# Performance work log

Measured on AMD Instinct MI355X. Metric: run time of the kernel, lower is better.

Reference implementation:

```python
import jax, jax.numpy as jnp
import numpy as np


def qdq(x):
    """Per-tensor symmetric int8 quantize-dequantize (act_quant + fp8_gemm dequant semantics)."""
    scale = jnp.maximum(jnp.max(jnp.abs(x)) / 127.0, 1e-8)
    q = jnp.clip(jnp.round(x / scale), -127.0, 127.0) * scale
    # straight-through estimator so the reference is also usable under autodiff
    return x + jax.lax.stop_gradient(q - x)


def layernorm(x, scale, bias, eps=1e-6):
    mean = jnp.mean(x, axis=-1, keepdims=True)
    var = jnp.mean(jnp.square(x - mean), axis=-1, keepdims=True)
    return (x - mean) * jax.lax.rsqrt(var + eps) * scale + bias


def glin(t, W, b):
    """TPUGEMMLinear: quantized GEMM (dequantized matmul) + bias."""
    return jnp.matmul(qdq(t), qdq(W)) + b


def setup_inputs() -> dict:
    key = jax.random.key(0)
    ks = jax.random.split(key, 12)
    B, S, D = 4, 1024, 1024
    H, HD, F, P = 32, 32, 4096, 32
    lecun = lambda k, shape: jax.random.normal(k, shape, jnp.float32) * (1.0 / np.sqrt(shape[0]))
    return {
        'inputs': jax.random.normal(ks[0], (B, S, D), jnp.float32),
        'ln1_scale': jnp.ones((D,), jnp.float32),
        'ln1_bias': jnp.zeros((D,), jnp.float32),
        'Wq': lecun(ks[1], (D, H * HD)), 'bq': jnp.zeros((H * HD,), jnp.float32),
        'Wk': lecun(ks[2], (D, H * HD)), 'bk': jnp.zeros((H * HD,), jnp.float32),
        'Wv': lecun(ks[3], (D, H * HD)), 'bv': jnp.zeros((H * HD,), jnp.float32),
        'rel_pos_emb': jax.random.normal(ks[4], (2 * P + 1, HD), jnp.float32) * 0.02,
        'Wo': lecun(ks[5], (H * HD, D)), 'bo': jnp.zeros((D,), jnp.float32),
        'ln2_scale': jnp.ones((D,), jnp.float32),
        'ln2_bias': jnp.zeros((D,), jnp.float32),
        'W1': lecun(ks[6], (D, F)), 'b1': jnp.zeros((F,), jnp.float32),
        'W2': lecun(ks[7], (F, D)), 'b2': jnp.zeros((D,), jnp.float32),
    }


def reference(inputs, ln1_scale, ln1_bias, Wq, bq, Wk, bk, Wv, bv, rel_pos_emb,
              Wo, bo, ln2_scale, ln2_bias, W1, b1, W2, b2):
    B, S, D = inputs.shape
    HD = rel_pos_emb.shape[1]
    H = D // HD
    P = (rel_pos_emb.shape[0] - 1) // 2

    # Pre-attention LayerNorm (TPULayerNorm, eps=1e-6)
    x = layernorm(inputs, ln1_scale, ln1_bias)

    # Quantized QKV projections
    q = glin(x, Wq, bq).reshape(B, S, H, HD).transpose(0, 2, 1, 3)  # [B,H,S,HD]
    k = glin(x, Wk, bk).reshape(B, S, H, HD).transpose(0, 2, 1, 3)
    v = glin(x, Wv, bv).reshape(B, S, H, HD).transpose(0, 2, 1, 3)

    # Relative position bias: [1, HD, S, S] broadcast onto head axis (HD == H by construction)
    pos = jnp.clip(jnp.arange(S)[:, None] - jnp.arange(S)[None, :] + P, 0, 2 * P)
    rel_bias = rel_pos_emb[pos].transpose(2, 0, 1)[None]  # [1, HD, S, S]

    # Quantized content scores + bias, custom scale factor
    scores = jnp.einsum('bhqd,bhkd->bhqk', qdq(q), qdq(k)) + rel_bias
    scale = jnp.sqrt(jnp.asarray(HD, jnp.float32)) * jnp.power(jnp.asarray(S, jnp.float32), 0.25)
    scores = scores / scale

    # Stable softmax with +1e-6 denominator (as in source)
    m = jnp.max(scores, axis=-1, keepdims=True)
    e = jnp.exp(scores - m)
    w = e / (jnp.sum(e, axis=-1, keepdims=True) + 1e-6)

    attn = jnp.einsum('bhqk,bhkd->bhqd', w, qdq(v))  # values quantized, weights not
    attn = attn.transpose(0, 2, 1, 3).reshape(B, S, H * HD)
    attn_out = glin(attn, Wo, bo)

    xr = attn_out + inputs
    y = layernorm(xr, ln2_scale, ln2_bias)

    # MLP (_mlp_tpu assumed: quantized Linear -> gelu -> quantized Linear)
    h = jax.nn.gelu(glin(y, W1, b1))
    out = glin(h, W2, b2)
    # NOTE: source returns mlp_output directly (no second residual add)
    return out
```

## Files before the change

### kernel.cpp

```cpp
#include <hip/hip_runtime.h>
#include <cstdint>


typedef unsigned short u16;
typedef __bf16 bf16x4 __attribute__((ext_vector_type(4)));
typedef __bf16 bf16x8 __attribute__((ext_vector_type(8)));
typedef float  f32x4  __attribute__((ext_vector_type(4)));

#define MFMA(a, b, c) __builtin_amdgcn_mfma_f32_16x16x32_bf16(a, b, c, 0, 0, 0)

#define NSLOT 13
#define PSPREAD 64
#define PSTRIDE 16
#define SLOTSZ (PSPREAD * PSTRIDE)

__device__ __forceinline__ float bf2f(u16 h) {
    return __uint_as_float(((unsigned)h) << 16);
}
__device__ __forceinline__ u16 f2bf(float f) {
    unsigned u = __float_as_uint(f);
    u += 0x7FFFu + ((u >> 16) & 1u);
    return (u16)(u >> 16);
}
__device__ __forceinline__ float qdqv(float v, float s) {
    float q = rintf(v / s);
    q = fminf(fmaxf(q, -127.f), 127.f);
    return q * s;
}

__device__ __forceinline__ float getscale64(const int* scales, int slot) {
    float m = __int_as_float(scales[slot * SLOTSZ + (threadIdx.x & 63) * PSTRIDE]);
#pragma unroll
    for (int o = 32; o > 0; o >>= 1) m = fmaxf(m, __shfl_xor(m, o));
    return fmaxf(m / 127.f, 1e-8f);
}

typedef const __attribute__((address_space(1))) unsigned gas_u32;
typedef __attribute__((address_space(3))) unsigned las_u32;
__device__ __forceinline__ void gld16(const void* g, void* l) {
    __builtin_amdgcn_global_load_lds((gas_u32*)g, (las_u32*)l, 16, 0, 0);
}

__global__ void zero_k(int* s) {
    const int i = blockIdx.x * 256 + threadIdx.x;
    if (i < NSLOT * SLOTSZ) s[i] = 0;
}

__global__ __launch_bounds__(256) void wabsmax6_k(const float* __restrict__ w0, const float* __restrict__ w1,
                                                  const float* __restrict__ w2, const float* __restrict__ w3,
                                                  const float* __restrict__ w4, const float* __restrict__ w5,
                                                  int* scales) {
    const int b = blockIdx.x;
    int ti, boff;
    if (b < 1024)      { ti = b >> 8; boff = (b & 255) * 4096; }
    else if (b < 2048) { ti = 4;      boff = (b - 1024) * 4096; }
    else               { ti = 5;      boff = (b - 2048) * 4096; }
    const float* w = (ti == 0) ? w0 : (ti == 1) ? w1 : (ti == 2) ? w2
                   : (ti == 3) ? w3 : (ti == 4) ? w4 : w5;
    const float4* wv = (const float4*)(w + boff);
    float m = 0.f;
#pragma unroll
    for (int k = 0; k < 4; k++) {
        float4 v = wv[threadIdx.x + k * 256];
        m = fmaxf(m, fmaxf(fmaxf(fabsf(v.x), fabsf(v.y)), fmaxf(fabsf(v.z), fabsf(v.w))));
    }
#pragma unroll
    for (int o = 32; o > 0; o >>= 1) m = fmaxf(m, __shfl_xor(m, o));
    if ((threadIdx.x & 63) == 0)
        atomicMax(scales + (7 + ti) * SLOTSZ + (((b * 4 + (threadIdx.x >> 6)) & (PSPREAD - 1)) * PSTRIDE),
                  __float_as_int(m));
}

__global__ __launch_bounds__(256) void wqt6_k(const float* __restrict__ w0, const float* __restrict__ w1,
                                              const float* __restrict__ w2, const float* __restrict__ w3,
                                              const float* __restrict__ w4, const float* __restrict__ w5,
                                              u16* __restrict__ wtbase, const int* __restrict__ scales) {
    __shared__ float t[32][33];
    const int b = blockIdx.x;
    const float* W;
    u16* Wt;
    int K, N, bx, by, slot;
    if (b < 4096) {
        const int ti = b >> 10, r = b & 1023;
        W = (ti == 0) ? w0 : (ti == 1) ? w1 : (ti == 2) ? w2 : w3;
        Wt = wtbase + (long)ti * 1048576;
        K = 1024; N = 1024; bx = r & 31; by = r >> 5; slot = 7 + ti;
    } else if (b < 8192) {
        const int r = b - 4096;
        W = w4; Wt = wtbase + 4194304;
        K = 1024; N = 4096; bx = r & 127; by = r >> 7; slot = 11;
    } else {
        const int r = b - 8192;
        W = w5; Wt = wtbase + 8388608;
        K = 4096; N = 1024; bx = r & 31; by = r >> 5; slot = 12;
    }
    const int n0 = bx * 32, k0 = by * 32;
    const float s = getscale64(scales, slot);
    const int c = threadIdx.x & 31, r0 = threadIdx.x >> 5;
#pragma unroll
    for (int i = 0; i < 4; i++) {
        int kk = k0 + r0 + i * 8;
        t[r0 + i * 8][c] = qdqv(W[(long)kk * N + n0 + c], s);
    }
    __syncthreads();
#pragma unroll
    for (int i = 0; i < 4; i++) {
        int nn = n0 + r0 + i * 8;
        Wt[(long)nn * K + k0 + c] = f2bf(t[c][r0 + i * 8]);
    }
}

__device__ __forceinline__ float blk_sum(float v, float* red) {
#pragma unroll
    for (int o = 32; o > 0; o >>= 1) v += __shfl_xor(v, o);
    __syncthreads();
    if ((threadIdx.x & 63) == 0) red[threadIdx.x >> 6] = v;
    __syncthreads();
    return red[0] + red[1] + red[2] + red[3];
}

__device__ __forceinline__ void blk_absmax_commit(float am, float* red, int* scales, int slot) {
#pragma unroll
    for (int o = 32; o > 0; o >>= 1) am = fmaxf(am, __shfl_xor(am, o));
    __syncthreads();
    if ((threadIdx.x & 63) == 0) red[threadIdx.x >> 6] = am;
    __syncthreads();
    if (threadIdx.x == 0) {
        float m = fmaxf(fmaxf(red[0], red[1]), fmaxf(red[2], red[3]));
        atomicMax(scales + slot * SLOTSZ + ((blockIdx.x & (PSPREAD - 1)) * PSTRIDE),
                  __float_as_int(m));
    }
}

__global__ __launch_bounds__(256) void ln_k(const float* __restrict__ in, const float* __restrict__ gam,
                                            const float* __restrict__ bet, u16* __restrict__ out,
                                            int* __restrict__ scales, int slot) {
    __shared__ float red[4];
    const long row = blockIdx.x;
    const int tid = threadIdx.x;
    float4 v = ((const float4*)(in + row * 1024))[tid];
    float mean = blk_sum(v.x + v.y + v.z + v.w, red) * (1.f / 1024.f);
    float dx = v.x - mean, dy = v.y - mean, dz = v.z - mean, dw = v.w - mean;
    float var = blk_sum(dx * dx + dy * dy + dz * dz + dw * dw, red) * (1.f / 1024.f);
    float inv = rsqrtf(var + 1e-6f);
    float4 gg = ((const float4*)gam)[tid];
    float4 bb = ((const float4*)bet)[tid];
    float o0 = dx * inv * gg.x + bb.x, o1 = dy * inv * gg.y + bb.y;
    float o2 = dz * inv * gg.z + bb.z, o3 = dw * inv * gg.w + bb.w;
    ushort4 st;
    st.x = f2bf(o0); st.y = f2bf(o1); st.z = f2bf(o2); st.w = f2bf(o3);
    ((ushort4*)(out + row * 1024))[tid] = st;
    float am = fmaxf(fmaxf(fabsf(o0), fabsf(o1)), fmaxf(fabsf(o2), fabsf(o3)));
    blk_absmax_commit(am, red, scales, slot);
}

__global__ __launch_bounds__(256) void ln2comb_k(const float* __restrict__ p, const float* __restrict__ bo,
                                                 const float* __restrict__ inputs,
                                                 const float* __restrict__ gam, const float* __restrict__ bet,
                                                 u16* __restrict__ out, int* __restrict__ scales) {
    __shared__ float red[4];
    const long row = blockIdx.x;
    const int tid = threadIdx.x;
    float4 a = ((const float4*)(p + row * 1024))[tid];
    float4 b = ((const float4*)(p + 4194304 + row * 1024))[tid];
    float4 bb0 = ((const float4*)bo)[tid];
    float4 xi = ((const float4*)(inputs + row * 1024))[tid];
    float4 v;
    v.x = a.x + b.x + bb0.x + xi.x; v.y = a.y + b.y + bb0.y + xi.y;
    v.z = a.z + b.z + bb0.z + xi.z; v.w = a.w + b.w + bb0.w + xi.w;
    float mean = blk_sum(v.x + v.y + v.z + v.w, red) * (1.f / 1024.f);
    float dx = v.x - mean, dy = v.y - mean, dz = v.z - mean, dw = v.w - mean;
    float var = blk_sum(dx * dx + dy * dy + dz * dz + dw * dw, red) * (1.f / 1024.f);
    float inv = rsqrtf(var + 1e-6f);
    float4 gg = ((const float4*)gam)[tid];
    float4 bb = ((const float4*)bet)[tid];
    float o0 = dx * inv * gg.x + bb.x, o1 = dy * inv * gg.y + bb.y;
    float o2 = dz * inv * gg.z + bb.z, o3 = dw * inv * gg.w + bb.w;
    ushort4 st;
    st.x = f2bf(o0); st.y = f2bf(o1); st.z = f2bf(o2); st.w = f2bf(o3);
    ((ushort4*)(out + row * 1024))[tid] = st;
    float am = fmaxf(fmaxf(fabsf(o0), fabsf(o1)), fmaxf(fabsf(o2), fabsf(o3)));
    blk_absmax_commit(am, red, scales, 5);
}

__global__ void combo_k(const float* __restrict__ p, const float* __restrict__ b2,
                        float* __restrict__ out) {
    const int i = blockIdx.x * 256 + threadIdx.x;
    float4 a = ((const float4*)p)[i];
    float4 b = ((const float4*)(p + 4194304))[i];
    float4 bb = ((const float4*)b2)[i & 255];
    float4 o;
    o.x = a.x + b.x + bb.x; o.y = a.y + b.y + bb.y;
    o.z = a.z + b.z + bb.z; o.w = a.w + b.w + bb.w;
    ((float4*)out)[i] = o;
}

__global__ void qact_k(u16* buf, int n8, const int* __restrict__ scales, int slot) {
    const float s = getscale64(scales, slot);
    int i = blockIdx.x * 256 + threadIdx.x;
    if (i >= n8) return;
    uint4 u = ((const uint4*)buf)[i];
    unsigned w[4] = {u.x, u.y, u.z, u.w};
#pragma unroll
    for (int j = 0; j < 4; j++) {
        float lo = qdqv(bf2f((u16)(w[j] & 0xFFFFu)), s);
        float hi = qdqv(bf2f((u16)(w[j] >> 16)), s);
        w[j] = (unsigned)f2bf(lo) | ((unsigned)f2bf(hi) << 16);
    }
    uint4 o; o.x = w[0]; o.y = w[1]; o.z = w[2]; o.w = w[3];
    ((uint4*)buf)[i] = o;
}

__global__ void qact2_k(u16* buf, const int* __restrict__ scales) {
    const int i = blockIdx.x * 256 + threadIdx.x;
    const int slot = (i >= 524288) ? 2 : 1;
    const float s = getscale64(scales, slot);
    uint4 u = ((const uint4*)buf)[i];
    unsigned w[4] = {u.x, u.y, u.z, u.w};
#pragma unroll
    for (int j = 0; j < 4; j++) {
        float lo = qdqv(bf2f((u16)(w[j] & 0xFFFFu)), s);
        float hi = qdqv(bf2f((u16)(w[j] >> 16)), s);
        w[j] = (unsigned)f2bf(lo) | ((unsigned)f2bf(hi) << 16);
    }
    uint4 o; o.x = w[0]; o.y = w[1]; o.z = w[2]; o.w = w[3];
    ((uint4*)buf)[i] = o;
}

__global__ __launch_bounds__(256) void vtrans_k(const u16* __restrict__ v, u16* __restrict__ vt,
                                                const int* __restrict__ scales) {
    __shared__ u16 t[32][33];
    const int bh = blockIdx.y, s0 = blockIdx.x * 32;
    const float s = getscale64(scales, 3);
    const int c = threadIdx.x & 31, r0 = threadIdx.x >> 5;
    const u16* src = v + ((long)bh * 1024 + s0) * 32;
#pragma unroll
    for (int i = 0; i < 4; i++) {
        int r = r0 + i * 8;
        t[r][c] = f2bf(qdqv(bf2f(src[r * 32 + c]), s));
    }
    __syncthreads();
    u16* dst = vt + (long)bh * 32768;
#pragma unroll
    for (int i = 0; i < 4; i++) {
        int r = r0 + i * 8;
        dst[(long)r * 1024 + s0 + c] = t[c][r];
    }
}

template <int EPI>
__global__ __launch_bounds__(256, 2) void gemm_k(const u16* __restrict__ A, const u16* __restrict__ Bt,
                                                 const float* __restrict__ bias, const float* __restrict__ bias2,
                                                 const float* __restrict__ bias3,
                                                 int M, int N, int Kfull, int Kslice,
                                                 float* __restrict__ outf, u16* __restrict__ outb,
                                                 int* __restrict__ scales, int slot) {
    __shared__ u16 As[128 * 64];
    __shared__ u16 Bs[128 * 64];
    const float* bp = bias;
    long koff = 0, ooff = 0;
    if (EPI == 0) {
        const int z = blockIdx.z;
        Bt += (long)z * 1048576;
        outb += (long)z * 4194304;
        bp = (z == 0) ? bias : (z == 1 ? bias2 : bias3);
        slot += z;
    }
    if (EPI == 4) {
        koff = (long)blockIdx.z * Kslice * 2;
        ooff = (long)blockIdx.z * M * N;
    }
    const int tid = threadIdx.x;
    const int lane = tid & 63;
    const int wave = tid >> 6;
    const int wm = wave >> 1, wn = wave & 1;
    const int bm = blockIdx.y * 128, bn = blockIdx.x * 128;
    const int g = lane >> 4, c = lane & 15;

    const long astride = (long)Kfull * 2;
    const int srow = wave * 32 + (lane >> 3);
    const int scol = ((lane & 7) * 16) ^ ((lane >> 3) << 4);
    const char* Ag = (const char*)A + (long)(bm + srow) * astride + scol + koff;
    const char* Bg = (const char*)Bt + (long)(bn + srow) * astride + scol + koff;
    char* Al = (char*)As + wave * 4096;
    char* Bl = (char*)Bs + wave * 4096;

    f32x4 acc[4][4];
    const f32x4 zf = {0.f, 0.f, 0.f, 0.f};
#pragma unroll
    for (int i = 0; i < 4; i++)
#pragma unroll
        for (int j = 0; j < 4; j++) acc[i][j] = zf;

    const int nk = Kslice >> 6;
    for (int kt = 0; kt < nk; ++kt) {
        __syncthreads();
        const long ko = (long)kt * 128;
#pragma unroll
        for (int i = 0; i < 4; i++) gld16(Ag + ko + (long)(i * 8) * astride, Al + i * 1024);
#pragma unroll
        for (int i = 0; i < 4; i++) gld16(Bg + ko + (long)(i * 8) * astride, Bl + i * 1024);
        __syncthreads();

#pragma unroll
        for (int kh = 0; kh < 2; kh++) {
            bf16x8 af[4], bq[4];
            const int kb = kh * 64 + g * 16;
            const int sw = kb ^ ((c & 7) << 4);
#pragma unroll
            for (int i = 0; i < 4; i++)
                af[i] = *(const bf16x8*)((const char*)As + (wm * 64 + i * 16 + c) * 128 + sw);
#pragma unroll
            for (int j = 0; j < 4; j++)
                bq[j] = *(const bf16x8*)((const char*)Bs + (wn * 64 + j * 16 + c) * 128 + sw);
#pragma unroll
            for (int i = 0; i < 4; i++)
#pragma unroll
                for (int j = 0; j < 4; j++)
                    acc[i][j] = MFMA(af[i], bq[j], acc[i][j]);
        }
    }

    float am = 0.f;
#pragma unroll
    for (int i = 0; i < 4; i++) {
#pragma unroll
        for (int j = 0; j < 4; j++) {
#pragma unroll
            for (int t = 0; t < 4; t++) {
                const int row = bm + wm * 64 + i * 16 + g * 4 + t;
                const int col = bn + wn * 64 + j * 16 + c;
                if (EPI == 0) {
                    float v = acc[i][j][t] + bp[col];
                    long oi = ((long)((row >> 10) * 32 + (col >> 5))) * 32768
                              + (long)(row & 1023) * 32 + (col & 31);
                    outb[oi] = f2bf(v);
                    am = fmaxf(am, fabsf(v));
                } else if (EPI == 2) {
                    float v = acc[i][j][t] + bp[col];
                    float t3 = v * v * v;
                    float gl = 0.5f * v * (1.f + tanhf(0.79788456080286536f * (v + 0.044715f * t3)));
                    outb[(long)row * N + col] = f2bf(gl);
                    am = fmaxf(am, fabsf(gl));
                } else {
                    outf[ooff + (long)row * N + col] = acc[i][j][t];
                }
            }
        }
    }
    if (EPI == 0 || EPI == 2) {
#pragma unroll
        for (int o = 32; o > 0; o >>= 1) am = fmaxf(am, __shfl_xor(am, o));
        if (lane == 0)
            atomicMax(scales + slot * SLOTSZ
                          + ((((blockIdx.x + blockIdx.y * gridDim.x) * 4 + wave) & (PSPREAD - 1)) * PSTRIDE),
                      __float_as_int(am));
    }
}

__global__ __launch_bounds__(256) void attn_k(const u16* __restrict__ q, const u16* __restrict__ k,
                                              const u16* __restrict__ vt, const float* __restrict__ relpos,
                                              u16* __restrict__ attn, int* __restrict__ scales) {
    __shared__ float rel_s[65];
    __shared__ u16 P[4][32 * 40];
    __shared__ float frs[4][32];
    const int tid = threadIdx.x;
    const int lane = tid & 63;
    const int w = tid >> 6;
    const int bh = blockIdx.x;
    const int b = bh >> 5, h = bh & 31;
    const int q0 = blockIdx.y * 128 + w * 32;
    const int g = lane >> 4, c = lane & 15;
    const float SC = 0.03125f;
    for (int i = tid; i < 65; i += 256) rel_s[i] = relpos[i * 32 + h] * SC;
    __syncthreads();
    const float rb0 = rel_s[0], rb64 = rel_s[64];

    const u16* qb = q + ((long)bh * 1024 + q0) * 32;
    const u16* kb = k + (long)bh * 32768;
    const u16* vb = vt + (long)bh * 32768;
    u16* Pw = P[w];
    float* fw = frs[w];

    bf16x8 aq[2];
#pragma unroll
    for (int i = 0; i < 2; i++) aq[i] = *(const bf16x8*)(qb + (i * 16 + c) * 32 + g * 8);

    const f32x4 zf = {0.f, 0.f, 0.f, 0.f};
    f32x4 o[2][2] = {{zf, zf}, {zf, zf}};
    float m_run[2] = {-1e30f, -1e30f};
    float l_run[2] = {0.f, 0.f};

    for (int kt = 0; kt < 32; ++kt) {
        const int kk = kt * 32;
        bf16x8 bk0 = *(const bf16x8*)(kb + (kk + c) * 32 + g * 8);
        bf16x8 bk1 = *(const bf16x8*)(kb + (kk + 16 + c) * 32 + g * 8);
        bf16x8 bv0 = *(const bf16x8*)(vb + c * 1024 + kk + g * 8);
        bf16x8 bv1 = *(const bf16x8*)(vb + (16 + c) * 1024 + kk + g * 8);
        const int mode = (kk >= q0 + 64) ? 0 : (kk <= q0 - 64) ? 1 : 2;

        float frv[2];
#pragma unroll
        for (int i = 0; i < 2; i++) {
            f32x4 s0 = MFMA(bk0, aq[i], zf);
            f32x4 s1 = MFMA(bk1, aq[i], zf);
            float v[8];
            if (mode == 0) {
#pragma unroll
                for (int t = 0; t < 4; t++) { v[t] = fmaf(s0[t], SC, rb0); v[4 + t] = fmaf(s1[t], SC, rb0); }
            } else if (mode == 1) {
#pragma unroll
                for (int t = 0; t < 4; t++) { v[t] = fmaf(s0[t], SC, rb64); v[4 + t] = fmaf(s1[t], SC, rb64); }
            } else {
                const int base = (q0 + i * 16 + c) - kk - g * 4 + 32;
#pragma unroll
                for (int t = 0; t < 4; t++) {
                    int d0 = min(max(base - t, 0), 64);
                    int d1 = min(max(base - 16 - t, 0), 64);
                    v[t] = fmaf(s0[t], SC, rel_s[d0]);
                    v[4 + t] = fmaf(s1[t], SC, rel_s[d1]);
                }
            }
            float mt = fmaxf(fmaxf(fmaxf(v[0], v[1]), fmaxf(v[2], v[3])),
                             fmaxf(fmaxf(v[4], v[5]), fmaxf(v[6], v[7])));
            mt = fmaxf(mt, __shfl_xor(mt, 16));
            mt = fmaxf(mt, __shfl_xor(mt, 32));
            const float mn = fmaxf(m_run[i], mt);
            const float fr = __expf(m_run[i] - mn);
            frv[i] = fr;
            float sm = 0.f;
            bf16x4 pk0, pk1;
#pragma unroll
            for (int t = 0; t < 4; t++) {
                float p = __expf(v[t] - mn);     sm += p; pk0[t] = (__bf16)p;
                float p2 = __expf(v[4 + t] - mn); sm += p2; pk1[t] = (__bf16)p2;
            }
            sm += __shfl_xor(sm, 16);
            sm += __shfl_xor(sm, 32);
            l_run[i] = l_run[i] * fr + sm;
            m_run[i] = mn;
            *(bf16x4*)&Pw[(i * 16 + c) * 40 + g * 4] = pk0;
            *(bf16x4*)&Pw[(i * 16 + c) * 40 + 16 + g * 4] = pk1;
        }
        if (__any((frv[0] != 1.f) | (frv[1] != 1.f))) {
            if (g == 0) { fw[c] = frv[0]; fw[16 + c] = frv[1]; }
            float4 f0 = *(float4*)&fw[g * 4];
            float4 f1 = *(float4*)&fw[16 + g * 4];
#pragma unroll
            for (int j = 0; j < 2; j++) {
                o[0][j][0] *= f0.x; o[0][j][1] *= f0.y; o[0][j][2] *= f0.z; o[0][j][3] *= f0.w;
                o[1][j][0] *= f1.x; o[1][j][1] *= f1.y; o[1][j][2] *= f1.z; o[1][j][3] *= f1.w;
            }
        }
        bf16x8 ap0 = *(const bf16x8*)&Pw[c * 40 + g * 8];
        bf16x8 ap1 = *(const bf16x8*)&Pw[(16 + c) * 40 + g * 8];
        o[0][0] = MFMA(ap0, bv0, o[0][0]);
        o[0][1] = MFMA(ap0, bv1, o[0][1]);
        o[1][0] = MFMA(ap1, bv0, o[1][0]);
        o[1][1] = MFMA(ap1, bv1, o[1][1]);
    }

    if (g == 0) { fw[c] = l_run[0]; fw[16 + c] = l_run[1]; }
    float4 l0 = *(float4*)&fw[g * 4];
    float4 l1 = *(float4*)&fw[16 + g * 4];
    float lv[2][4] = {{l0.x, l0.y, l0.z, l0.w}, {l1.x, l1.y, l1.z, l1.w}};
    float am = 0.f;
#pragma unroll
    for (int i = 0; i < 2; i++)
#pragma unroll
        for (int j = 0; j < 2; j++)
#pragma unroll
            for (int t = 0; t < 4; t++) {
                float val = o[i][j][t] / (lv[i][t] + 1e-6f);
                long row = (long)b * 1024 + q0 + i * 16 + g * 4 + t;
                attn[row * 1024 + h * 32 + j * 16 + c] = f2bf(val);
                am = fmaxf(am, fabsf(val));
            }
#pragma unroll
    for (int o2 = 32; o2 > 0; o2 >>= 1) am = fmaxf(am, __shfl_xor(am, o2));
    if (lane == 0)
        atomicMax(scales + 4 * SLOTSZ + ((((bh * 8 + blockIdx.y) * 4 + w) & (PSPREAD - 1)) * PSTRIDE),
                  __float_as_int(am));
}

extern "C" void kernel_launch(void* const* d_in, const int* in_sizes, int n_in,
                              void* d_out, int out_size, void* d_ws, size_t ws_size,
                              hipStream_t stream) {
    (void)in_sizes; (void)n_in; (void)out_size; (void)ws_size;
    const float* inputs = (const float*)d_in[0];
    const float* ln1s   = (const float*)d_in[1];
    const float* ln1b   = (const float*)d_in[2];
    const float* Wq     = (const float*)d_in[3];
    const float* bq     = (const float*)d_in[4];
    const float* Wk     = (const float*)d_in[5];
    const float* bk     = (const float*)d_in[6];
    const float* Wv     = (const float*)d_in[7];
    const float* bv     = (const float*)d_in[8];
    const float* rel    = (const float*)d_in[9];
    const float* Wo     = (const float*)d_in[10];
    const float* bo     = (const float*)d_in[11];
    const float* ln2s   = (const float*)d_in[12];
    const float* ln2b   = (const float*)d_in[13];
    const float* W1     = (const float*)d_in[14];
    const float* b1     = (const float*)d_in[15];
    const float* W2     = (const float*)d_in[16];
    const float* b2     = (const float*)d_in[17];
    float* out = (float*)d_out;

    char* ws = (char*)d_ws;
    int* scales = (int*)ws;
    char* regionA = ws + 65536;
    char* regionB = regionA + (32u << 20);
    char* regionC = regionB + (32u << 20);
    u16* qb    = (u16*)regionA;
    u16* kbuf  = qb + 4194304;
    u16* vbuf  = kbuf + 4194304;
    u16* vtb   = vbuf + 4194304;
    float* pWo = (float*)regionA;
    u16* hb    = (u16*)regionA;
    u16* xq    = (u16*)regionB;
    u16* attnb = xq;
    u16* yb    = xq + 4194304;
    float* pW2 = (float*)regionB;
    u16* wtb   = (u16*)regionC;

    zero_k<<<52, 256, 0, stream>>>(scales);
    wabsmax6_k<<<3072, 256, 0, stream>>>(Wq, Wk, Wv, Wo, W1, W2, scales);

    ln_k<<<4096, 256, 0, stream>>>(inputs, ln1s, ln1b, xq, scales, 0);

    wqt6_k<<<12288, 256, 0, stream>>>(Wq, Wk, Wv, Wo, W1, W2, wtb, scales);

    qact_k<<<2048, 256, 0, stream>>>(xq, 524288, scales, 0);

    gemm_k<0><<<dim3(8, 32, 3), 256, 0, stream>>>(xq, wtb, bq, bk, bv, 4096, 1024, 1024, 1024,
                                                  nullptr, qb, scales, 1);

    qact2_k<<<4096, 256, 0, stream>>>(qb, scales);
    vtrans_k<<<dim3(32, 128), 256, 0, stream>>>(vbuf, vtb, scales);

    attn_k<<<dim3(128, 8), 256, 0, stream>>>(qb, kbuf, vtb, rel, attnb, scales);
    qact_k<<<2048, 256, 0, stream>>>(attnb, 524288, scales, 4);

    gemm_k<4><<<dim3(8, 32, 2), 256, 0, stream>>>(attnb, wtb + 3145728, nullptr, nullptr, nullptr,
                                                  4096, 1024, 1024, 512, pWo, nullptr, scales, -1);
    ln2comb_k<<<4096, 256, 0, stream>>>(pWo, bo, inputs, ln2s, ln2b, yb, scales);
    qact_k<<<2048, 256, 0, stream>>>(yb, 524288, scales, 5);

    gemm_k<2><<<dim3(32, 32), 256, 0, stream>>>(yb, wtb + 4194304, b1, nullptr, nullptr,
                                                4096, 4096, 1024, 1024, nullptr, hb, scales, 6);
    qact_k<<<8192, 256, 0, stream>>>(hb, 2097152, scales, 6);

    gemm_k<4><<<dim3(8, 32, 2), 256, 0, stream>>>(hb, wtb + 8388608, nullptr, nullptr, nullptr,
                                                  4096, 1024, 4096, 2048, pW2, nullptr, scales, -1);
    combo_k<<<4096, 256, 0, stream>>>(pW2, b2, out);
}
```

Baseline: 315.6 us.

## Fuse small prologue kernels, split W2 GEMM four ways, shrink attention row tiles

Merges the weight-absmax kernel with the LN1 kernel, and the Q/K requantize kernel with the V quantize-transpose kernel, to cut launch count and tail effects. Splits the final W2 GEMM into four K-slices instead of two. The extra partial sums go to freed workspace and to the output buffer, and the combine kernel sums all four. Attention now gives each wave 16 query rows instead of 32 and launches twice as many blocks with a higher occupancy hint. This raises parallelism but halves K/V reuse per wave and adds more loads per MFMA.

Measured after the change: 345.2 us. 9.4% more time.

```diff
diff --git a/kernel.cpp b/kernel.cpp
--- a/kernel.cpp
+++ b/kernel.cpp
@@ -46,29 +46,74 @@
     if (i < NSLOT * SLOTSZ) s[i] = 0;
 }
 
-__global__ __launch_bounds__(256) void wabsmax6_k(const float* __restrict__ w0, const float* __restrict__ w1,
-                                                  const float* __restrict__ w2, const float* __restrict__ w3,
-                                                  const float* __restrict__ w4, const float* __restrict__ w5,
-                                                  int* scales) {
-    const int b = blockIdx.x;
-    int ti, boff;
-    if (b < 1024)      { ti = b >> 8; boff = (b & 255) * 4096; }
-    else if (b < 2048) { ti = 4;      boff = (b - 1024) * 4096; }
-    else               { ti = 5;      boff = (b - 2048) * 4096; }
-    const float* w = (ti == 0) ? w0 : (ti == 1) ? w1 : (ti == 2) ? w2
-                   : (ti == 3) ? w3 : (ti == 4) ? w4 : w5;
-    const float4* wv = (const float4*)(w + boff);
-    float m = 0.f;
-#pragma unroll
-    for (int k = 0; k < 4; k++) {
-        float4 v = wv[threadIdx.x + k * 256];
-        m = fmaxf(m, fmaxf(fmaxf(fabsf(v.x), fabsf(v.y)), fmaxf(fabsf(v.z), fabsf(v.w))));
-    }
-#pragma unroll
-    for (int o = 32; o > 0; o >>= 1) m = fmaxf(m, __shfl_xor(m, o));
-    if ((threadIdx.x & 63) == 0)
-        atomicMax(scales + (7 + ti) * SLOTSZ + (((b * 4 + (threadIdx.x >> 6)) & (PSPREAD - 1)) * PSTRIDE),
+__device__ __forceinline__ float blk_sum(float v, float* red) {
+#pragma unroll
+    for (int o = 32; o > 0; o >>= 1) v += __shfl_xor(v, o);
+    __syncthreads();
+    if ((threadIdx.x & 63) == 0) red[threadIdx.x >> 6] = v;
+    __syncthreads();
+    return red[0] + red[1] + red[2] + red[3];
+}
+
+__device__ __forceinline__ void blk_absmax_commit(float am, float* red, int* scales,
+                                                  int slot, int bidx) {
+#pragma unroll
+    for (int o = 32; o > 0; o >>= 1) am = fmaxf(am, __shfl_xor(am, o));
+    __syncthreads();
+    if ((threadIdx.x & 63) == 0) red[threadIdx.x >> 6] = am;
+    __syncthreads();
+    if (threadIdx.x == 0) {
+        float m = fmaxf(fmaxf(red[0], red[1]), fmaxf(red[2], red[3]));
+        atomicMax(scales + slot * SLOTSZ + ((bidx & (PSPREAD - 1)) * PSTRIDE),
                   __float_as_int(m));
+    }
+}
+
+__global__ __launch_bounds__(256) void waln_k(const float* __restrict__ w0, const float* __restrict__ w1,
+                                              const float* __restrict__ w2, const float* __restrict__ w3,
+                                              const float* __restrict__ w4, const float* __restrict__ w5,
+                                              const float* __restrict__ in, const float* __restrict__ gam,
+                                              const float* __restrict__ bet, u16* __restrict__ out,
+                                              int* __restrict__ scales) {
+    __shared__ float red[4];
+    const int tid = threadIdx.x;
+    if (blockIdx.x < 3072) {
+        const int b = blockIdx.x;
+        int ti, boff;
+        if (b < 1024)      { ti = b >> 8; boff = (b & 255) * 4096; }
+        else if (b < 2048) { ti = 4;      boff = (b - 1024) * 4096; }
+        else               { ti = 5;      boff = (b - 2048) * 4096; }
+        const float* w = (ti == 0) ? w0 : (ti == 1) ? w1 : (ti == 2) ? w2
+                       : (ti == 3) ? w3 : (ti == 4) ? w4 : w5;
+        const float4* wv = (const float4*)(w + boff);
+        float m = 0.f;
+#pragma unroll
+        for (int k = 0; k < 4; k++) {
+            float4 v = wv[tid + k * 256];
+            m = fmaxf(m, fmaxf(fmaxf(fabsf(v.x), fabsf(v.y)), fmaxf(fabsf(v.z), fabsf(v.w))));
+        }
+#pragma unroll
+        for (int o = 32; o > 0; o >>= 1) m = fmaxf(m, __shfl_xor(m, o));
+        if ((tid & 63) == 0)
+            atomicMax(scales + (7 + ti) * SLOTSZ + (((b * 4 + (tid >> 6)) & (PSPREAD - 1)) * PSTRIDE),
+                      __float_as_int(m));
+        return;
+    }
+    const long row = blockIdx.x - 3072;
+    float4 v = ((const float4*)(in + row * 1024))[tid];
+    float mean = blk_sum(v.x + v.y + v.z + v.w, red) * (1.f / 1024.f);
+    float dx = v.x - mean, dy = v.y - mean, dz = v.z - mean, dw = v.w - mean;
+    float var = blk_sum(dx * dx + dy * dy + dz * dz + dw * dw, red) * (1.f / 1024.f);
+    float inv = rsqrtf(var + 1e-6f);
+    float4 gg = ((const float4*)gam)[tid];
+    float4 bb = ((const float4*)bet)[tid];
+    float o0 = dx * inv * gg.x + bb.x, o1 = dy * inv * gg.y + bb.y;
+    float o2 = dz * inv * gg.z + bb.z, o3 = dw * inv * gg.w + bb.w;
+    ushort4 st;
+    st.x = f2bf(o0); st.y = f2bf(o1); st.z = f2bf(o2); st.w = f2bf(o3);
+    ((ushort4*)(out + row * 1024))[tid] = st;
+    float am = fmaxf(fmaxf(fabsf(o0), fabsf(o1)), fmaxf(fabsf(o2), fabsf(o3)));
+    blk_absmax_commit(am, red, scales, 0, (int)row);
 }
 
 __global__ __launch_bounds__(256) void wqt6_k(const float* __restrict__ w0, const float* __restrict__ w1,
@@ -108,50 +153,6 @@
         int nn = n0 + r0 + i * 8;
         Wt[(long)nn * K + k0 + c] = f2bf(t[c][r0 + i * 8]);
     }
-}
-
-__device__ __forceinline__ float blk_sum(float v, float* red) {
-#pragma unroll
-    for (int o = 32; o > 0; o >>= 1) v += __shfl_xor(v, o);
-    __syncthreads();
-    if ((threadIdx.x & 63) == 0) red[threadIdx.x >> 6] = v;
-    __syncthreads();
-    return red[0] + red[1] + red[2] + red[3];
-}
-
-__device__ __forceinline__ void blk_absmax_commit(float am, float* red, int* scales, int slot) {
-#pragma unroll
-    for (int o = 32; o > 0; o >>= 1) am = fmaxf(am, __shfl_xor(am, o));
-    __syncthreads();
-    if ((threadIdx.x & 63) == 0) red[threadIdx.x >> 6] = am;
-    __syncthreads();
-    if (threadIdx.x == 0) {
-        float m = fmaxf(fmaxf(red[0], red[1]), fmaxf(red[2], red[3]));
-        atomicMax(scales + slot * SLOTSZ + ((blockIdx.x & (PSPREAD - 1)) * PSTRIDE),
-                  __float_as_int(m));
-    }
-}
-
-__global__ __launch_bounds__(256) void ln_k(const float* __restrict__ in, const float* __restrict__ gam,
-                                            const float* __restrict__ bet, u16* __restrict__ out,
-                                            int* __restrict__ scales, int slot) {
-    __shared__ float red[4];
-    const long row = blockIdx.x;
-    const int tid = threadIdx.x;
-    float4 v = ((const float4*)(in + row * 1024))[tid];
-    float mean = blk_sum(v.x + v.y + v.z + v.w, red) * (1.f / 1024.f);
-    float dx = v.x - mean, dy = v.y - mean, dz = v.z - mean, dw = v.w - mean;
-    float var = blk_sum(dx * dx + dy * dy + dz * dz + dw * dw, red) * (1.f / 1024.f);
-    float inv = rsqrtf(var + 1e-6f);
-    float4 gg = ((const float4*)gam)[tid];
-    float4 bb = ((const float4*)bet)[tid];
-    float o0 = dx * inv * gg.x + bb.x, o1 = dy * inv * gg.y + bb.y;
-    float o2 = dz * inv * gg.z + bb.z, o3 = dw * inv * gg.w + bb.w;
-    ushort4 st;
-    st.x = f2bf(o0); st.y = f2bf(o1); st.z = f2bf(o2); st.w = f2bf(o3);
-    ((ushort4*)(out + row * 1024))[tid] = st;
-    float am = fmaxf(fmaxf(fabsf(o0), fabsf(o1)), fmaxf(fabsf(o2), fabsf(o3)));
-    blk_absmax_commit(am, red, scales, slot);
 }
 
 __global__ __launch_bounds__(256) void ln2comb_k(const float* __restrict__ p, const float* __restrict__ bo,
@@ -180,18 +181,22 @@
     st.x = f2bf(o0); st.y = f2bf(o1); st.z = f2bf(o2); st.w = f2bf(o3);
     ((ushort4*)(out + row * 1024))[tid] = st;
     float am = fmaxf(fmaxf(fabsf(o0), fabsf(o1)), fmaxf(fabsf(o2), fabsf(o3)));
-    blk_absmax_commit(am, red, scales, 5);
-}
-
-__global__ void combo_k(const float* __restrict__ p, const float* __restrict__ b2,
-                        float* __restrict__ out) {
+    blk_absmax_commit(am, red, scales, 5, (int)row);
+}
+
+__global__ void combo_k(const float* __restrict__ pa, const float* __restrict__ pc,
+                        const float* __restrict__ b2, float* __restrict__ out) {
     const int i = blockIdx.x * 256 + threadIdx.x;
-    float4 a = ((const float4*)p)[i];
-    float4 b = ((const float4*)(p + 4194304))[i];
+    float4 a0 = ((const float4*)pa)[i];
+    float4 a1 = ((const float4*)(pa + 4194304))[i];
+    float4 c0 = ((const float4*)pc)[i];
+    float4 c1 = ((const float4*)out)[i];
     float4 bb = ((const float4*)b2)[i & 255];
     float4 o;
-    o.x = a.x + b.x + bb.x; o.y = a.y + b.y + bb.y;
-    o.z = a.z + b.z + bb.z; o.w = a.w + b.w + bb.w;
+    o.x = ((a0.x + a1.x) + (c0.x + c1.x)) + bb.x;
+    o.y = ((a0.y + a1.y) + (c0.y + c1.y)) + bb.y;
+    o.z = ((a0.z + a1.z) + (c0.z + c1.z)) + bb.z;
+    o.w = ((a0.w + a1.w) + (c0.w + c1.w)) + bb.w;
     ((float4*)out)[i] = o;
 }
 
@@ -211,40 +216,42 @@
     ((uint4*)buf)[i] = o;
 }
 
-__global__ void qact2_k(u16* buf, const int* __restrict__ scales) {
-    const int i = blockIdx.x * 256 + threadIdx.x;
-    const int slot = (i >= 524288) ? 2 : 1;
-    const float s = getscale64(scales, slot);
-    uint4 u = ((const uint4*)buf)[i];
-    unsigned w[4] = {u.x, u.y, u.z, u.w};
-#pragma unroll
-    for (int j = 0; j < 4; j++) {
-        float lo = qdqv(bf2f((u16)(w[j] & 0xFFFFu)), s);
-        float hi = qdqv(bf2f((u16)(w[j] >> 16)), s);
-        w[j] = (unsigned)f2bf(lo) | ((unsigned)f2bf(hi) << 16);
-    }
-    uint4 o; o.x = w[0]; o.y = w[1]; o.z = w[2]; o.w = w[3];
-    ((uint4*)buf)[i] = o;
-}
-
-__global__ __launch_bounds__(256) void vtrans_k(const u16* __restrict__ v, u16* __restrict__ vt,
-                                                const int* __restrict__ scales) {
+__global__ __launch_bounds__(256) void vq_k(u16* __restrict__ qk, const u16* __restrict__ v,
+                                            u16* __restrict__ vt, const int* __restrict__ scales) {
     __shared__ u16 t[32][33];
-    const int bh = blockIdx.y, s0 = blockIdx.x * 32;
+    const int tid = threadIdx.x;
+    if (blockIdx.x < 4096) {
+        const int i = blockIdx.x * 256 + tid;
+        const int slot = (i >= 524288) ? 2 : 1;
+        const float s = getscale64(scales, slot);
+        uint4 u = ((const uint4*)qk)[i];
+        unsigned w[4] = {u.x, u.y, u.z, u.w};
+#pragma unroll
+        for (int j = 0; j < 4; j++) {
+            float lo = qdqv(bf2f((u16)(w[j] & 0xFFFFu)), s);
+            float hi = qdqv(bf2f((u16)(w[j] >> 16)), s);
+            w[j] = (unsigned)f2bf(lo) | ((unsigned)f2bf(hi) << 16);
+        }
+        uint4 o; o.x = w[0]; o.y = w[1]; o.z = w[2]; o.w = w[3];
+        ((uint4*)qk)[i] = o;
+        return;
+    }
+    const int r = blockIdx.x - 4096;
+    const int bh = r >> 5, s0 = (r & 31) * 32;
     const float s = getscale64(scales, 3);
-    const int c = threadIdx.x & 31, r0 = threadIdx.x >> 5;
+    const int c = tid & 31, r0 = tid >> 5;
     const u16* src = v + ((long)bh * 1024 + s0) * 32;
 #pragma unroll
     for (int i = 0; i < 4; i++) {
-        int r = r0 + i * 8;
-        t[r][c] = f2bf(qdqv(bf2f(src[r * 32 + c]), s));
+        int rr = r0 + i * 8;
+        t[rr][c] = f2bf(qdqv(bf2f(src[rr * 32 + c]), s));
     }
     __syncthreads();
     u16* dst = vt + (long)bh * 32768;
 #pragma unroll
     for (int i = 0; i < 4; i++) {
-        int r = r0 + i * 8;
-        dst[(long)r * 1024 + s0 + c] = t[c][r];
+        int rr = r0 + i * 8;
+        dst[(long)rr * 1024 + s0 + c] = t[c][rr];
     }
 }
 
@@ -253,12 +260,14 @@
                                                  const float* __restrict__ bias, const float* __restrict__ bias2,
                                                  const float* __restrict__ bias3,
                                                  int M, int N, int Kfull, int Kslice,
-                                                 float* __restrict__ outf, u16* __restrict__ outb,
+                                                 float* __restrict__ outf, float* __restrict__ outf2,
+                                                 float* __restrict__ outf3, u16* __restrict__ outb,
                                                  int* __restrict__ scales, int slot) {
     __shared__ u16 As[128 * 64];
     __shared__ u16 Bs[128 * 64];
     const float* bp = bias;
     long koff = 0, ooff = 0;
+    float* po = outf;
     if (EPI == 0) {
         const int z = blockIdx.z;
         Bt += (long)z * 1048576;
@@ -267,8 +276,11 @@
         slot += z;
     }
     if (EPI == 4) {
-        koff = (long)blockIdx.z * Kslice * 2;
-        ooff = (long)blockIdx.z * M * N;
+        const int z = blockIdx.z;
+        koff = (long)z * Kslice * 2;
+        if (z < 2)       { po = outf;  ooff = (long)z * M * N; }
+        else if (z == 2) { po = outf2; ooff = 0; }
+        else             { po = outf3; ooff = 0; }
     }
     const int tid = threadIdx.x;
     const int lane = tid & 63;
@@ -343,7 +355,7 @@
                     outb[(long)row * N + col] = f2bf(gl);
                     am = fmaxf(am, fabsf(gl));
                 } else {
-                    outf[ooff + (long)row * N + col] = acc[i][j][t];
+                    po[ooff + (long)row * N + col] = acc[i][j][t];
                 }
             }
         }
@@ -358,18 +370,18 @@
     }
 }
 
-__global__ __launch_bounds__(256) void attn_k(const u16* __restrict__ q, const u16* __restrict__ k,
-                                              const u16* __restrict__ vt, const float* __restrict__ relpos,
-                                              u16* __restrict__ attn, int* __restrict__ scales) {
+__global__ __launch_bounds__(256, 8) void attn_k(const u16* __restrict__ q, const u16* __restrict__ k,
+                                                 const u16* __restrict__ vt, const float* __restrict__ relpos,
+                                                 u16* __restrict__ attn, int* __restrict__ scales) {
     __shared__ float rel_s[65];
-    __shared__ u16 P[4][32 * 40];
-    __shared__ float frs[4][32];
+    __shared__ __align__(16) u16 P[4][16 * 40];
+    __shared__ float frs[4][16];
     const int tid = threadIdx.x;
     const int lane = tid & 63;
     const int w = tid >> 6;
     const int bh = blockIdx.x;
     const int b = bh >> 5, h = bh & 31;
-    const int q0 = blockIdx.y * 128 + w * 32;
+    const int q0 = (blockIdx.y * 4 + w) * 16;
     const int g = lane >> 4, c = lane & 15;
     const float SC = 0.03125f;
     for (int i = tid; i < 65; i += 256) rel_s[i] = relpos[i * 32 + h] * SC;
@@ -382,14 +394,11 @@
     u16* Pw = P[w];
     float* fw = frs[w];
 
-    bf16x8 aq[2];
-#pragma unroll
-    for (int i = 0; i < 2; i++) aq[i] = *(const bf16x8*)(qb + (i * 16 + c) * 32 + g * 8);
+    bf16x8 aq = *(const bf16x8*)(qb + c * 32 + g * 8);
 
     const f32x4 zf = {0.f, 0.f, 0.f, 0.f};
-    f32x4 o[2][2] = {{zf, zf}, {zf, zf}};
-    float m_run[2] = {-1e30f, -1e30f};
-    float l_run[2] = {0.f, 0.f};
+    f32x4 o0 = zf, o1 = zf;
+    float m_run = -1e30f, l_run = 0.f;
 
     for (int kt = 0; kt < 32; ++kt) {
         const int kk = kt * 32;
@@ -397,89 +406,75 @@
         bf16x8 bk1 = *(const bf16x8*)(kb + (kk + 16 + c) * 32 + g * 8);
         bf16x8 bv0 = *(const bf16x8*)(vb + c * 1024 + kk + g * 8);
         bf16x8 bv1 = *(const bf16x8*)(vb + (16 + c) * 1024 + kk + g * 8);
-        const int mode = (kk >= q0 + 64) ? 0 : (kk <= q0 - 64) ? 1 : 2;
-
-        float frv[2];
-#pragma unroll
-        for (int i = 0; i < 2; i++) {
-            f32x4 s0 = MFMA(bk0, aq[i], zf);
-            f32x4 s1 = MFMA(bk1, aq[i], zf);
-            float v[8];
-            if (mode == 0) {
-#pragma unroll
-                for (int t = 0; t < 4; t++) { v[t] = fmaf(s0[t], SC, rb0); v[4 + t] = fmaf(s1[t], SC, rb0); }
-            } else if (mode == 1) {
-#pragma unroll
-                for (int t = 0; t < 4; t++) { v[t] = fmaf(s0[t], SC, rb64); v[4 + t] = fmaf(s1[t], SC, rb64); }
-            } else {
-                const int base = (q0 + i * 16 + c) - kk - g * 4 + 32;
-#pragma unroll
-                for (int t = 0; t < 4; t++) {
-                    int d0 = min(max(base - t, 0), 64);
-                    int d1 = min(max(base - 16 - t, 0), 64);
-                    v[t] = fmaf(s0[t], SC, rel_s[d0]);
-                    v[4 + t] = fmaf(s1[t], SC, rel_s[d1]);
-                }
+        const int mode = (kk >= q0 + 48) ? 0 : (kk <= q0 - 64) ? 1 : 2;
+
+        f32x4 s0 = MFMA(bk0, aq, zf);
+        f32x4 s1 = MFMA(bk1, aq, zf);
+        float v[8];
+        if (mode == 0) {
+#pragma unroll
+            for (int t = 0; t < 4; t++) { v[t] = fmaf(s0[t], SC, rb0); v[4 + t] = fmaf(s1[t], SC, rb0); }
+        } else if (mode == 1) {
+#pragma unroll
+            for (int t = 0; t < 4; t++) { v[t] = fmaf(s0[t], SC, rb64); v[4 + t] = fmaf(s1[t], SC, rb64); }
+        } else {
+            const int base = (q0 + c) - kk - g * 4 + 32;
+#pragma unroll
+            for (int t = 0; t < 4; t++) {
+                int d0 = min(max(base - t, 0), 64);
+                int d1 = min(max(base - 16 - t, 0), 64);
+                v[t] = fmaf(s0[t], SC, rel_s[d0]);
+                v[4 + t] = fmaf(s1[t], SC, rel_s[d1]);
             }
-            float mt = fmaxf(fmaxf(fmaxf(v[0], v[1]), fmaxf(v[2], v[3])),
-                             fmaxf(fmaxf(v[4], v[5]), fmaxf(v[6], v[7])));
-            mt = fmaxf(mt, __shfl_xor(mt, 16));
-            mt = fmaxf(mt, __shfl_xor(mt, 32));
-            const float mn = fmaxf(m_run[i], mt);
-            const float fr = __expf(m_run[i] - mn);
-            frv[i] = fr;
-            float sm = 0.f;
-            bf16x4 pk0, pk1;
-#pragma unroll
-            for (int t = 0; t < 4; t++) {
-                float p = __expf(v[t] - mn);     sm += p; pk0[t] = (__bf16)p;
-                float p2 = __expf(v[4 + t] - mn); sm += p2; pk1[t] = (__bf16)p2;
-            }
-            sm += __shfl_xor(sm, 16);
-            sm += __shfl_xor(sm, 32);
-            l_run[i] = l_run[i] * fr + sm;
-            m_run[i] = mn;
-            *(bf16x4*)&Pw[(i * 16 + c) * 40 + g * 4] = pk0;
-            *(bf16x4*)&Pw[(i * 16 + c) * 40 + 16 + g * 4] = pk1;
-        }
-        if (__any((frv[0] != 1.f) | (frv[1] != 1.f))) {
-            if (g == 0) { fw[c] = frv[0]; fw[16 + c] = frv[1]; }
+        }
+        float mt = fmaxf(fmaxf(fmaxf(v[0], v[1]), fmaxf(v[2], v[3])),
+                         fmaxf(fmaxf(v[4], v[5]), fmaxf(v[6], v[7])));
+        mt = fmaxf(mt, __shfl_xor(mt, 16));
+        mt = fmaxf(mt, __shfl_xor(mt, 32));
+        const float mn = fmaxf(m_run, mt);
+        const float fr = __expf(m_run - mn);
+        float sm = 0.f;
+        bf16x4 pk0, pk1;
+#pragma unroll
+        for (int t = 0; t < 4; t++) {
+            float p = __expf(v[t] - mn);     sm += p; pk0[t] = (__bf16)p;
+            float p2 = __expf(v[4 + t] - mn); sm += p2; pk1[t] = (__bf16)p2;
+        }
+        sm += __shfl_xor(sm, 16);
+        sm += __shfl_xor(sm, 32);
+        l_run = l_run * fr + sm;
+        m_run = mn;
+        *(bf16x4*)&Pw[c * 40 + g * 4] = pk0;
+        *(bf16x4*)&Pw[c * 40 + 16 + g * 4] = pk1;
+
+        if (__any(fr != 1.f)) {
+            if (g == 0) fw[c] = fr;
             float4 f0 = *(float4*)&fw[g * 4];
-            float4 f1 = *(float4*)&fw[16 + g * 4];
-#pragma unroll
-            for (int j = 0; j < 2; j++) {
-                o[0][j][0] *= f0.x; o[0][j][1] *= f0.y; o[0][j][2] *= f0.z; o[0][j][3] *= f0.w;
-                o[1][j][0] *= f1.x; o[1][j][1] *= f1.y; o[1][j][2] *= f1.z; o[1][j][3] *= f1.w;
-            }
-        }
-        bf16x8 ap0 = *(const bf16x8*)&Pw[c * 40 + g * 8];
-        bf16x8 ap1 = *(const bf16x8*)&Pw[(16 + c) * 40 + g * 8];
-        o[0][0] = MFMA(ap0, bv0, o[0][0]);
-        o[0][1] = MFMA(ap0, bv1, o[0][1]);
-        o[1][0] = MFMA(ap1, bv0, o[1][0]);
-        o[1][1] = MFMA(ap1, bv1, o[1][1]);
-    }
-
-    if (g == 0) { fw[c] = l_run[0]; fw[16 + c] = l_run[1]; }
+            o0[0] *= f0.x; o0[1] *= f0.y; o0[2] *= f0.z; o0[3] *= f0.w;
+            o1[0] *= f0.x; o1[1] *= f0.y; o1[2] *= f0.z; o1[3] *= f0.w;
+        }
+        bf16x8 ap = *(const bf16x8*)&Pw[c * 40 + g * 8];
+        o0 = MFMA(ap, bv0, o0);
+        o1 = MFMA(ap, bv1, o1);
+    }
+
+    if (g == 0) fw[c] = l_run;
     float4 l0 = *(float4*)&fw[g * 4];
-    float4 l1 = *(float4*)&fw[16 + g * 4];
-    float lv[2][4] = {{l0.x, l0.y, l0.z, l0.w}, {l1.x, l1.y, l1.z, l1.w}};
+    float lv[4] = {l0.x, l0.y, l0.z, l0.w};
     float am = 0.f;
 #pragma unroll
-    for (int i = 0; i < 2; i++)
-#pragma unroll
-        for (int j = 0; j < 2; j++)
-#pragma unroll
-            for (int t = 0; t < 4; t++) {
-                float val = o[i][j][t] / (lv[i][t] + 1e-6f);
-                long row = (long)b * 1024 + q0 + i * 16 + g * 4 + t;
-                attn[row * 1024 + h * 32 + j * 16 + c] = f2bf(val);
-                am = fmaxf(am, fabsf(val));
-            }
+    for (int t = 0; t < 4; t++) {
+        const long row = (long)b * 1024 + q0 + g * 4 + t;
+        float v0 = o0[t] / (lv[t] + 1e-6f);
+        float v1 = o1[t] / (lv[t] + 1e-6f);
+        attn[row * 1024 + h * 32 + c] = f2bf(v0);
+        attn[row * 1024 + h * 32 + 16 + c] = f2bf(v1);
+        am = fmaxf(am, fmaxf(fabsf(v0), fabsf(v1)));
+    }
 #pragma unroll
     for (int o2 = 32; o2 > 0; o2 >>= 1) am = fmaxf(am, __shfl_xor(am, o2));
     if (lane == 0)
-        atomicMax(scales + 4 * SLOTSZ + ((((bh * 8 + blockIdx.y) * 4 + w) & (PSPREAD - 1)) * PSTRIDE),
+        atomicMax(scales + 4 * SLOTSZ + ((((bh * 16 + blockIdx.y) * 4 + w) & (PSPREAD - 1)) * PSTRIDE),
                   __float_as_int(am));
 }
 
@@ -521,37 +516,38 @@
     u16* xq    = (u16*)regionB;
     u16* attnb = xq;
     u16* yb    = xq + 4194304;
-    float* pW2 = (float*)regionB;
+    float* pW2  = (float*)regionB;
+    float* pW2c = (float*)regionC;
     u16* wtb   = (u16*)regionC;
 
     zero_k<<<52, 256, 0, stream>>>(scales);
-    wabsmax6_k<<<3072, 256, 0, stream>>>(Wq, Wk, Wv, Wo, W1, W2, scales);
-
-    ln_k<<<4096, 256, 0, stream>>>(inputs, ln1s, ln1b, xq, scales, 0);
+    waln_k<<<7168, 256, 0, stream>>>(Wq, Wk, Wv, Wo, W1, W2, inputs, ln1s, ln1b, xq, scales);
 
     wqt6_k<<<12288, 256, 0, stream>>>(Wq, Wk, Wv, Wo, W1, W2, wtb, scales);
 
     qact_k<<<2048, 256, 0, stream>>>(xq, 524288, scales, 0);
 
     gemm_k<0><<<dim3(8, 32, 3), 256, 0, stream>>>(xq, wtb, bq, bk, bv, 4096, 1024, 1024, 1024,
-                                                  nullptr, qb, scales, 1);
-
-    qact2_k<<<4096, 256, 0, stream>>>(qb, scales);
-    vtrans_k<<<dim3(32, 128), 256, 0, stream>>>(vbuf, vtb, scales);
-
-    attn_k<<<dim3(128, 8), 256, 0, stream>>>(qb, kbuf, vtb, rel, attnb, scales);
+                                                  nullptr, nullptr, nullptr, qb, scales, 1);
+
+    vq_k<<<8192, 256, 0, stream>>>(qb, vbuf, vtb, scales);
+
+    attn_k<<<dim3(128, 16), 256, 0, stream>>>(qb, kbuf, vtb, rel, attnb, scales);
     qact_k<<<2048, 256, 0, stream>>>(attnb, 524288, scales, 4);
 
     gemm_k<4><<<dim3(8, 32, 2), 256, 0, stream>>>(attnb, wtb + 3145728, nullptr, nullptr, nullptr,
-                                                  4096, 1024, 1024, 512, pWo, nullptr, scales, -1);
+                                                  4096, 1024, 1024, 512, pWo, nullptr, nullptr, nullptr,
+                                                  scales, -1);
     ln2comb_k<<<4096, 256, 0, stream>>>(pWo, bo, inputs, ln2s, ln2b, yb, scales);
     qact_k<<<2048, 256, 0, stream>>>(yb, 524288, scales, 5);
 
     gemm_k<2><<<dim3(32, 32), 256, 0, stream>>>(yb, wtb + 4194304, b1, nullptr, nullptr,
-                                                4096, 4096, 1024, 1024, nullptr, hb, scales, 6);
+                                                4096, 4096, 1024, 1024, nullptr, nullptr, nullptr, hb,
+                                                scales, 6);
     qact_k<<<8192, 256, 0, stream>>>(hb, 2097152, scales, 6);
 
-    gemm_k<4><<<dim3(8, 32, 2), 256, 0, stream>>>(hb, wtb + 8388608, nullptr, nullptr, nullptr,
-                                                  4096, 1024, 4096, 2048, pW2, nullptr, scales, -1);
-    combo_k<<<4096, 256, 0, stream>>>(pW2, b2, out);
-}
+    gemm_k<4><<<dim3(8, 32, 4), 256, 0, stream>>>(hb, wtb + 8388608, nullptr, nullptr, nullptr,
+                                                  4096, 1024, 4096, 1024, pW2, pW2c, out, nullptr,
+                                                  scales, -1);
+    combo_k<<<4096, 256, 0, stream>>>(pW2, pW2c, b2, out);
+}
```
